# Performance work log

Measured on AMD Instinct MI355X. Metric: run time of the kernel, lower is better.

The kernel has to match this reference:

```python
import jax, jax.numpy as jnp
from jax import lax
import numpy as np

MAX_VAL = 255.0
LEVELS = 5
MS_WEIGHTS = np.array([0.0448, 0.2856, 0.3001, 0.2363, 0.1333], dtype=np.float32)


def _gaussian_window(window_size: int, sigma: float) -> jnp.ndarray:
    # 1D gaussian -> outer product -> [1, 1, ws, ws] conv kernel (channel=1 depthwise)
    x = np.arange(window_size, dtype=np.float64)
    g = np.exp(-((x - window_size // 2) ** 2) / (2.0 * sigma ** 2))
    g = (g / g.sum()).astype(np.float32)
    w2d = np.outer(g, g)
    return jnp.asarray(w2d[None, None, :, :])


def _conv_same(x, win, pad):
    return lax.conv_general_dilated(
        x, win, window_strides=(1, 1), padding=[(pad, pad), (pad, pad)],
        dimension_numbers=('NCHW', 'OIHW', 'NCHW'))


def _ssim_level(img1, img2):
    _, _, w, h = img1.shape
    window_size = min(w, h, 11)
    sigma = 1.5 * window_size / 11
    win = _gaussian_window(window_size, sigma)
    pad = window_size // 2

    mu1 = _conv_same(img1, win, pad)
    mu2 = _conv_same(img2, win, pad)
    mu1_sq = mu1 * mu1
    mu2_sq = mu2 * mu2
    mu1_mu2 = mu1 * mu2
    sigma1_sq = _conv_same(img1 * img1, win, pad) - mu1_sq
    sigma2_sq = _conv_same(img2 * img2, win, pad) - mu2_sq
    sigma12 = _conv_same(img1 * img2, win, pad) - mu1_mu2

    C1 = (0.01 * MAX_VAL) ** 2
    C2 = (0.03 * MAX_VAL) ** 2
    V1 = 2.0 * sigma12 + C2
    V2 = sigma1_sq + sigma2_sq + C2
    ssim_map = (2.0 * mu1_mu2 + C1) * V1 / ((mu1_sq + mu2_sq + C1) * V2)
    mcs_map = V1 / V2
    return ssim_map.mean(), mcs_map.mean()


def _avg_pool2(x):
    b, c, h, w = x.shape
    return x.reshape(b, c, h // 2, 2, w // 2, 2).mean(axis=(3, 5))


def _ms_ssim(img1, img2):
    msssim = []
    mcs = []
    for _ in range(LEVELS):
        s, m = _ssim_level(img1, img2)
        msssim.append(s)
        mcs.append(m)
        img1 = _avg_pool2(img1)
        img2 = _avg_pool2(img2)
    weight = jnp.asarray(MS_WEIGHTS)
    mcs = jnp.stack(mcs)
    value = jnp.prod(mcs[:LEVELS - 1] ** weight[:LEVELS - 1]) * msssim[-1] ** weight[LEVELS - 1]
    return jnp.clip(value / 2.0, 0.0, 1.0)


def setup_inputs() -> dict:
    key = jax.random.key(0)
    k1, k2 = jax.random.split(key)
    shape = (16, 1, 512, 512)
    img1 = jax.random.uniform(k1, shape, dtype=jnp.float32)
    img2 = jax.random.uniform(k2, shape, dtype=jnp.float32)
    return {"img1": img1, "img2": img2}


def reference(img1, img2):
    return _ms_ssim(img1, img2)
```

## Files before the change

### kernel.cpp

```cpp
#include <hip/hip_runtime.h>
#include <hip/hip_fp16.h>
#include <math.h>


#define WS 11
#define TW 64
#define TH 32
#define SROWS 42
#define HSTRIDE 68

__device__ __forceinline__ void gauss_weights(float* w) {
    float s = 0.f;
#pragma unroll
    for (int j = 0; j < WS; ++j) {
        float d = (float)(j - 5);
        float e = expf(-d * d / 4.5f);
        w[j] = e;
        s += e;
    }
    float inv = 1.f / s;
#pragma unroll
    for (int j = 0; j < WS; ++j) w[j] *= inv;
}

__device__ __forceinline__ void h_task(
    int t, const float* __restrict__ p1, const float* __restrict__ p2,
    int W, int x0, int y0, bool interior, const float* w,
    __half2* __restrict__ hSD, __half2* __restrict__ hQ)
{
    int r = t >> 4, xg = t & 15;
    int gy = y0 - 5 + r;
    int gxb = x0 - 8 + 4 * xg;
    float fs[20], fd[20];
    if (interior) {
        const float* r1p = p1 + (size_t)gy * W + gxb;
        const float* r2p = p2 + (size_t)gy * W + gxb;
#pragma unroll
        for (int k = 0; k < 5; ++k) {
            float4 a = *(const float4*)(r1p + 4 * k);
            float4 c = *(const float4*)(r2p + 4 * k);
            fs[4 * k]     = a.x + c.x;  fd[4 * k]     = a.x - c.x;
            fs[4 * k + 1] = a.y + c.y;  fd[4 * k + 1] = a.y - c.y;
            fs[4 * k + 2] = a.z + c.z;  fd[4 * k + 2] = a.z - c.z;
            fs[4 * k + 3] = a.w + c.w;  fd[4 * k + 3] = a.w - c.w;
        }
    } else if (gy >= 0 && gy < W) {
        const float* r1p = p1 + (size_t)gy * W;
        const float* r2p = p2 + (size_t)gy * W;
#pragma unroll
        for (int k = 0; k < 5; ++k) {
            int gx = gxb + 4 * k;
            float4 a = make_float4(0.f, 0.f, 0.f, 0.f);
            float4 c = make_float4(0.f, 0.f, 0.f, 0.f);
            if (gx >= 0 && gx + 3 < W) {
                a = *(const float4*)(r1p + gx);
                c = *(const float4*)(r2p + gx);
            } else if (gx + 3 >= 0 && gx < W) {
                float t1[4] = {0.f, 0.f, 0.f, 0.f};
                float t2[4] = {0.f, 0.f, 0.f, 0.f};
#pragma unroll
                for (int u = 0; u < 4; ++u) {
                    int gxx = gx + u;
                    if (gxx >= 0 && gxx < W) { t1[u] = r1p[gxx]; t2[u] = r2p[gxx]; }
                }
                a = make_float4(t1[0], t1[1], t1[2], t1[3]);
                c = make_float4(t2[0], t2[1], t2[2], t2[3]);
            }
            fs[4 * k]     = a.x + c.x;  fd[4 * k]     = a.x - c.x;
            fs[4 * k + 1] = a.y + c.y;  fd[4 * k + 1] = a.y - c.y;
            fs[4 * k + 2] = a.z + c.z;  fd[4 * k + 2] = a.z - c.z;
            fs[4 * k + 3] = a.w + c.w;  fd[4 * k + 3] = a.w - c.w;
        }
    } else {
#pragma unroll
        for (int k = 0; k < 20; ++k) { fs[k] = 0.f; fd[k] = 0.f; }
    }
    float qs[14], qd[14];
#pragma unroll
    for (int k = 0; k < 14; ++k) {
        qs[k] = fs[k + 3] * fs[k + 3];
        qd[k] = fd[k + 3] * fd[k + 3];
    }
    __half2 outSD[4], outQ[4];
#pragma unroll
    for (int c = 0; c < 4; ++c) {
        float aS = 0.f, aD = 0.f, aS2 = 0.f, aD2 = 0.f;
#pragma unroll
        for (int j = 0; j < WS; ++j) {
            float wj = w[j];
            aS  = fmaf(wj, fs[3 + c + j], aS);
            aD  = fmaf(wj, fd[3 + c + j], aD);
            aS2 = fmaf(wj, qs[c + j], aS2);
            aD2 = fmaf(wj, qd[c + j], aD2);
        }
        outSD[c] = __float22half2_rn(make_float2(aS, aD));
        outQ[c]  = __float22half2_rn(make_float2(aS2, aD2));
    }
    int ho = r * HSTRIDE + 4 * xg;
    *(float4*)&hSD[ho] = *(const float4*)outSD;
    *(float4*)&hQ[ho]  = *(const float4*)outQ;
}

__device__ __forceinline__ void v_phase(
    int W, int x0, int y0, const float* w,
    const __half2* __restrict__ hSD, const __half2* __restrict__ hQ,
    float red[2][4], float* __restrict__ partials, int part_idx)
{
    const int tid = threadIdx.x;
    const int x = tid & 15;
    const int g = tid >> 4;
    float accS[2][4], accD[2][4], accS2[2][4], accD2[2][4];
#pragma unroll
    for (int rr = 0; rr < 2; ++rr)
#pragma unroll
        for (int c = 0; c < 4; ++c) {
            accS[rr][c] = 0.f; accD[rr][c] = 0.f;
            accS2[rr][c] = 0.f; accD2[rr][c] = 0.f;
        }

#pragma unroll
    for (int r = 0; r < 12; ++r) {
        int ho = (2 * g + r) * HSTRIDE + 4 * x;
        float4 rawSD = *(const float4*)&hSD[ho];
        float4 rawQ  = *(const float4*)&hQ[ho];
        const __half2* hpSD = (const __half2*)&rawSD;
        const __half2* hpQ  = (const __half2*)&rawQ;
        float lS[4], lD[4], lS2[4], lD2[4];
#pragma unroll
        for (int c = 0; c < 4; ++c) {
            float2 sd = __half22float2(hpSD[c]);
            float2 q  = __half22float2(hpQ[c]);
            lS[c] = sd.x; lD[c] = sd.y; lS2[c] = q.x; lD2[c] = q.y;
        }
        if (r < 11) {
            float wv = w[r];
#pragma unroll
            for (int c = 0; c < 4; ++c) {
                accS[0][c]  = fmaf(wv, lS[c],  accS[0][c]);
                accD[0][c]  = fmaf(wv, lD[c],  accD[0][c]);
                accS2[0][c] = fmaf(wv, lS2[c], accS2[0][c]);
                accD2[0][c] = fmaf(wv, lD2[c], accD2[0][c]);
            }
        }
        if (r >= 1) {
            float wv = w[r - 1];
#pragma unroll
            for (int c = 0; c < 4; ++c) {
                accS[1][c]  = fmaf(wv, lS[c],  accS[1][c]);
                accD[1][c]  = fmaf(wv, lD[c],  accD[1][c]);
                accS2[1][c] = fmaf(wv, lS2[c], accS2[1][c]);
                accD2[1][c] = fmaf(wv, lD2[c], accD2[1][c]);
            }
        }
    }

    const float C1 = 6.5025f;
    const float C2 = 58.5225f;
    const int Hv = min(TH, W - y0);
    const int Wv = min(TW, W - x0);
    float sacc = 0.f, macc = 0.f;
#pragma unroll
    for (int rr = 0; rr < 2; ++rr) {
        int row = 2 * g + rr;
#pragma unroll
        for (int c = 0; c < 4; ++c) {
            float ms = accS[rr][c], md = accD[rr][c];
            float es = accS2[rr][c], ed = accD2[rr][c];
            float ms2 = ms * ms, md2 = md * md;
            float a  = 0.5f * (ms2 - md2);
            float bb = 0.5f * (ms2 + md2);
            float pq = 0.5f * (es - ed);
            float qq = 0.5f * (es + ed);
            float V1 = (pq - a) + C2;
            float V2 = (qq - bb) + C2;
            float num = a + C1;
            float den = bb + C1;
            float inv = 1.0f / (den * V2);
            float sv = num * V1 * inv;
            float mv = V1 * den * inv;
            if (row < Hv && (4 * x + c) < Wv) { sacc += sv; macc += mv; }
        }
    }

#pragma unroll
    for (int o = 32; o > 0; o >>= 1) {
        sacc += __shfl_down(sacc, o);
        macc += __shfl_down(macc, o);
    }
    int wave = tid >> 6, lane = tid & 63;
    if (lane == 0) { red[0][wave] = sacc; red[1][wave] = macc; }
    __syncthreads();
    if (tid == 0) {
        float s = red[0][0] + red[0][1] + red[0][2] + red[0][3];
        float m = red[1][0] + red[1][1] + red[1][2] + red[1][3];
        partials[2 * part_idx] = s;
        partials[2 * part_idx + 1] = m;
    }
}

__global__ __launch_bounds__(256) void ssim_l0_pool_kernel(
    const float* __restrict__ img1, const float* __restrict__ img2,
    float* __restrict__ l1a, float* __restrict__ l1b,
    float* __restrict__ l2a, float* __restrict__ l2b,
    float* __restrict__ l3a, float* __restrict__ l3b,
    float* __restrict__ l4a, float* __restrict__ l4b,
    float* __restrict__ partials)
{
    __shared__ __half2 hSD[SROWS * HSTRIDE];
    __shared__ __half2 hQ[SROWS * HSTRIDE];
    __shared__ float pl1a[16 * 36];
    __shared__ float pl1b[16 * 36];
    __shared__ float red[2][4];

    const int tid = threadIdx.x;
    const int tx = blockIdx.x, ty = blockIdx.y, b = blockIdx.z;
    const int x0 = tx * TW, y0 = ty * TH;
    const float* p1 = img1 + (size_t)b * 512 * 512;
    const float* p2 = img2 + (size_t)b * 512 * 512;

    float w[WS];
    gauss_weights(w);

    const bool interior = (x0 >= 8) && (x0 <= 512 - 72) && (y0 >= 5) && (y0 <= 512 - 37);

#pragma unroll 1
    for (int t = tid; t < SROWS * 16; t += 256)
        h_task(t, p1, p2, 512, x0, y0, interior, w, hSD, hQ);

#pragma unroll 1
    for (int q = 0; q < 2; ++q) {
        int t = tid + q * 256;
        int r = t >> 5, c = t & 31;
        int gy = y0 + 2 * r, gx = x0 + 2 * c;
        const float* a0 = p1 + (size_t)gy * 512 + gx;
        const float* c0 = p2 + (size_t)gy * 512 + gx;
        float2 u0 = *(const float2*)a0;
        float2 u1 = *(const float2*)(a0 + 512);
        float2 t0 = *(const float2*)c0;
        float2 t1 = *(const float2*)(c0 + 512);
        float v1 = 0.25f * ((u0.x + u0.y) + (u1.x + u1.y));
        float v2 = 0.25f * ((t0.x + t0.y) + (t1.x + t1.y));
        size_t o1 = (size_t)b * 256 * 256 + (size_t)(y0 / 2 + r) * 256 + (x0 / 2 + c);
        l1a[o1] = v1;
        l1b[o1] = v2;
        pl1a[r * 36 + c] = v1;
        pl1b[r * 36 + c] = v2;
    }
    __syncthreads();

    if (tid < 64) {
        int lane = tid;
#pragma unroll
        for (int t = lane; t < 128; t += 64) {
            int r = t >> 4, c = t & 15;
            int R = 2 * r, C = 2 * c;
            float v1 = 0.25f * ((pl1a[R * 36 + C] + pl1a[R * 36 + C + 1]) +
                                (pl1a[(R + 1) * 36 + C] + pl1a[(R + 1) * 36 + C + 1]));
            float v2 = 0.25f * ((pl1b[R * 36 + C] + pl1b[R * 36 + C + 1]) +
                                (pl1b[(R + 1) * 36 + C] + pl1b[(R + 1) * 36 + C + 1]));
            size_t o = (size_t)b * 128 * 128 + (size_t)(y0 / 4 + r) * 128 + (x0 / 4 + c);
            l2a[o] = v1;
            l2b[o] = v2;
        }
        if (lane < 32) {
            int r = lane >> 3, c = lane & 7;
            float q1[2][2], q2[2][2];
#pragma unroll
            for (int i = 0; i < 2; ++i)
#pragma unroll
                for (int j = 0; j < 2; ++j) {
                    int R = 4 * r + 2 * i, C = 4 * c + 2 * j;
                    q1[i][j] = 0.25f * ((pl1a[R * 36 + C] + pl1a[R * 36 + C + 1]) +
                                        (pl1a[(R + 1) * 36 + C] + pl1a[(R + 1) * 36 + C + 1]));
                    q2[i][j] = 0.25f * ((pl1b[R * 36 + C] + pl1b[R * 36 + C + 1]) +
                                        (pl1b[(R + 1) * 36 + C] + pl1b[(R + 1) * 36 + C + 1]));
                }
            float v1 = 0.25f * ((q1[0][0] + q1[0][1]) + (q1[1][0] + q1[1][1]));
            float v2 = 0.25f * ((q2[0][0] + q2[0][1]) + (q2[1][0] + q2[1][1]));
            size_t o = (size_t)b * 64 * 64 + (size_t)(y0 / 8 + r) * 64 + (x0 / 8 + c);
            l3a[o] = v1;
            l3b[o] = v2;
        }
        if (lane < 8) {
            int r = lane >> 2, c = lane & 3;
            float p3a[2][2], p3b[2][2];
#pragma unroll
            for (int i3 = 0; i3 < 2; ++i3)
#pragma unroll
                for (int j3 = 0; j3 < 2; ++j3) {
                    float p2a[2][2], p2b[2][2];
#pragma unroll
                    for (int i2 = 0; i2 < 2; ++i2)
#pragma unroll
                        for (int j2 = 0; j2 < 2; ++j2) {
                            int R = 8 * r + 4 * i3 + 2 * i2;
                            int C = 8 * c + 4 * j3 + 2 * j2;
                            p2a[i2][j2] = 0.25f * ((pl1a[R * 36 + C] + pl1a[R * 36 + C + 1]) +
                                                   (pl1a[(R + 1) * 36 + C] + pl1a[(R + 1) * 36 + C + 1]));
                            p2b[i2][j2] = 0.25f * ((pl1b[R * 36 + C] + pl1b[R * 36 + C + 1]) +
                                                   (pl1b[(R + 1) * 36 + C] + pl1b[(R + 1) * 36 + C + 1]));
                        }
                    p3a[i3][j3] = 0.25f * ((p2a[0][0] + p2a[0][1]) + (p2a[1][0] + p2a[1][1]));
                    p3b[i3][j3] = 0.25f * ((p2b[0][0] + p2b[0][1]) + (p2b[1][0] + p2b[1][1]));
                }
            float v1 = 0.25f * ((p3a[0][0] + p3a[0][1]) + (p3a[1][0] + p3a[1][1]));
            float v2 = 0.25f * ((p3b[0][0] + p3b[0][1]) + (p3b[1][0] + p3b[1][1]));
            size_t o = (size_t)b * 32 * 32 + (size_t)(y0 / 16 + r) * 32 + (x0 / 16 + c);
            l4a[o] = v1;
            l4b[o] = v2;
        }
    }

    int part_idx = ((b * 16 + ty) * 8) + tx;
    v_phase(512, x0, y0, w, hSD, hQ, red, partials, part_idx);
}

__global__ __launch_bounds__(256) void ssim_rest_kernel(
    const float* __restrict__ l1a, const float* __restrict__ l1b,
    const float* __restrict__ l2a, const float* __restrict__ l2b,
    const float* __restrict__ l3a, const float* __restrict__ l3b,
    const float* __restrict__ l4a, const float* __restrict__ l4b,
    float* __restrict__ partials)
{
    __shared__ __half2 hSD[SROWS * HSTRIDE];
    __shared__ __half2 hQ[SROWS * HSTRIDE];
    __shared__ float red[2][4];

    const int tid = threadIdx.x;
    const int lin = blockIdx.x;
    int level, base;
    if (lin < 512)      { level = 1; base = 0; }
    else if (lin < 640) { level = 2; base = 512; }
    else if (lin < 672) { level = 3; base = 640; }
    else                { level = 4; base = 672; }
    const int Wt[4]   = {256, 128, 64, 32};
    const int ntxl[4] = {2, 1, 0, 0};
    const int ntyl[4] = {3, 2, 1, 0};
    const int idx = level - 1;
    const int W = Wt[idx];
    const int li = lin - base;
    const int tx = li & ((1 << ntxl[idx]) - 1);
    const int rem = li >> ntxl[idx];
    const int ty = rem & ((1 << ntyl[idx]) - 1);
    const int b = rem >> ntyl[idx];

    const float* ip1; const float* ip2;
    if (level == 1)      { ip1 = l1a; ip2 = l1b; }
    else if (level == 2) { ip1 = l2a; ip2 = l2b; }
    else if (level == 3) { ip1 = l3a; ip2 = l3b; }
    else                 { ip1 = l4a; ip2 = l4b; }
    const float* p1 = ip1 + (size_t)b * W * W;
    const float* p2 = ip2 + (size_t)b * W * W;

    const int x0 = tx * TW, y0 = ty * TH;

    float w[WS];
    gauss_weights(w);

    const bool interior = (x0 >= 8) && (x0 <= W - 72) && (y0 >= 5) && (y0 <= W - 37);

#pragma unroll 1
    for (int t = tid; t < SROWS * 16; t += 256)
        h_task(t, p1, p2, W, x0, y0, interior, w, hSD, hQ);
    __syncthreads();

    v_phase(W, x0, y0, w, hSD, hQ, red, partials, lin);
}

__global__ __launch_bounds__(256) void finalize_kernel(
    const float* __restrict__ partials, float* __restrict__ out)
{
    __shared__ float lvl_s[5], lvl_m[5];
    __shared__ float red[2][4];
    const int nb[5] = {2048, 512, 128, 32, 16};
    const int off[5] = {0, 2048, 2560, 2688, 2720};
    const float npix[5] = {16.f * 512 * 512, 16.f * 256 * 256, 16.f * 128 * 128,
                           16.f * 64 * 64, 16.f * 32 * 32};
    const int tid = threadIdx.x;

    for (int l = 0; l < 5; ++l) {
        float s = 0.f, m = 0.f;
        for (int i = tid; i < nb[l]; i += 256) {
            s += partials[2 * (off[l] + i)];
            m += partials[2 * (off[l] + i) + 1];
        }
#pragma unroll
        for (int o = 32; o > 0; o >>= 1) {
            s += __shfl_down(s, o);
            m += __shfl_down(m, o);
        }
        int wave = tid >> 6, lane = tid & 63;
        if (lane == 0) { red[0][wave] = s; red[1][wave] = m; }
        __syncthreads();
        if (tid == 0) {
            lvl_s[l] = (red[0][0] + red[0][1] + red[0][2] + red[0][3]) / npix[l];
            lvl_m[l] = (red[1][0] + red[1][1] + red[1][2] + red[1][3]) / npix[l];
        }
        __syncthreads();
    }

    if (tid == 0) {
        const float w[5] = {0.0448f, 0.2856f, 0.3001f, 0.2363f, 0.1333f};
        float v = powf(lvl_m[0], w[0]) * powf(lvl_m[1], w[1]) * powf(lvl_m[2], w[2]) *
                  powf(lvl_m[3], w[3]) * powf(lvl_s[4], w[4]);
        v *= 0.5f;
        v = fminf(fmaxf(v, 0.f), 1.f);
        out[0] = v;
    }
}

extern "C" void kernel_launch(void* const* d_in, const int* in_sizes, int n_in,
                              void* d_out, int out_size, void* d_ws, size_t ws_size,
                              hipStream_t stream) {
    const float* img1 = (const float*)d_in[0];
    const float* img2 = (const float*)d_in[1];
    float* out = (float*)d_out;

    const int B = 16;

    float* wsf = (float*)d_ws;
    float* partials = wsf;
    float* p = wsf + 5472;
    float* l1a = p; p += (size_t)B * 256 * 256;
    float* l1b = p; p += (size_t)B * 256 * 256;
    float* l2a = p; p += (size_t)B * 128 * 128;
    float* l2b = p; p += (size_t)B * 128 * 128;
    float* l3a = p; p += (size_t)B * 64 * 64;
    float* l3b = p; p += (size_t)B * 64 * 64;
    float* l4a = p; p += (size_t)B * 32 * 32;
    float* l4b = p; p += (size_t)B * 32 * 32;

    dim3 block(256);

    ssim_l0_pool_kernel<<<dim3(8, 16, B), block, 0, stream>>>(
        img1, img2, l1a, l1b, l2a, l2b, l3a, l3b, l4a, l4b, partials);

    ssim_rest_kernel<<<dim3(688), block, 0, stream>>>(
        l1a, l1b, l2a, l2b, l3a, l3b, l4a, l4b, partials + 2 * 2048);

    finalize_kernel<<<1, block, 0, stream>>>(partials, out);
}
```

Measured before the change: 130.5 us.

## Stage input halo tiles into LDS with direct global-to-LDS loads

```diff
diff --git a/kernel.cpp b/kernel.cpp
--- a/kernel.cpp
+++ b/kernel.cpp
@@ -7,7 +7,14 @@
 #define TW 64
 #define TH 32
 #define SROWS 42
-#define HSTRIDE 68
+#define SSTRIDE 80
+#define SFLOATS (SROWS * SSTRIDE)
+#define SALLOC 3584
+#define HSTRIDE 64
+#define PL1S 34
+
+typedef const __attribute__((address_space(1))) void gvoid_t;
+typedef __attribute__((address_space(3))) void lvoid_t;
 
 __device__ __forceinline__ void gauss_weights(float* w) {
     float s = 0.f;
@@ -23,57 +30,64 @@
     for (int j = 0; j < WS; ++j) w[j] *= inv;
 }
 
+__device__ __forceinline__ void stage_tile(
+    const float* __restrict__ g1, const float* __restrict__ g2,
+    int H, int W, int x0, int y0,
+    float* __restrict__ s1, float* __restrict__ s2, int tid)
+{
+    const int lane = tid & 63;
+    const int wave = tid >> 6;
+    for (int c = wave; c < 14; c += 4) {
+        int f = c * 256 + lane * 4;
+        int row = f / 80;
+        int col = f - row * 80;
+        int gy = y0 - 5 + row;
+        gy = max(0, min(H - 1, gy));
+        int gx = x0 - 8 + col;
+        gx = max(0, min(W - 4, gx));
+        const float* p1 = g1 + (size_t)gy * W + gx;
+        const float* p2 = g2 + (size_t)gy * W + gx;
+        __builtin_amdgcn_global_load_lds((gvoid_t*)p1, (lvoid_t*)(s1 + f), 16, 0, 0);
+        __builtin_amdgcn_global_load_lds((gvoid_t*)p2, (lvoid_t*)(s2 + f), 16, 0, 0);
+    }
+}
+
+__device__ __forceinline__ void zero_fix(
+    int H, int W, int x0, int y0,
+    float* __restrict__ s1, float* __restrict__ s2, int tid)
+{
+    bool anyOOB = (y0 < 5) || (y0 + 37 > H) || (x0 < 8) || (x0 + 72 > W);
+    if (anyOOB) {
+        for (int t = tid; t < SFLOATS; t += 256) {
+            int r = t / 80, c = t - (t / 80) * 80;
+            int gy = y0 - 5 + r, gx = x0 - 8 + c;
+            if (gy < 0 || gy >= H || gx < 0 || gx >= W) {
+                s1[t] = 0.f;
+                s2[t] = 0.f;
+            }
+        }
+    }
+}
+
 __device__ __forceinline__ void h_task(
-    int t, const float* __restrict__ p1, const float* __restrict__ p2,
-    int W, int x0, int y0, bool interior, const float* w,
-    __half2* __restrict__ hSD, __half2* __restrict__ hQ)
+    int t, const float* __restrict__ s1, const float* __restrict__ s2,
+    const float* w, __half2* __restrict__ hSD, __half2* __restrict__ hQ)
 {
     int r = t >> 4, xg = t & 15;
-    int gy = y0 - 5 + r;
-    int gxb = x0 - 8 + 4 * xg;
+    int sb = r * SSTRIDE + 4 * xg;
+    float f1[20], f2[20];
+#pragma unroll
+    for (int k = 0; k < 5; ++k) {
+        float4 a = *(const float4*)&s1[sb + 4 * k];
+        float4 c = *(const float4*)&s2[sb + 4 * k];
+        f1[4 * k] = a.x; f1[4 * k + 1] = a.y; f1[4 * k + 2] = a.z; f1[4 * k + 3] = a.w;
+        f2[4 * k] = c.x; f2[4 * k + 1] = c.y; f2[4 * k + 2] = c.z; f2[4 * k + 3] = c.w;
+    }
     float fs[20], fd[20];
-    if (interior) {
-        const float* r1p = p1 + (size_t)gy * W + gxb;
-        const float* r2p = p2 + (size_t)gy * W + gxb;
-#pragma unroll
-        for (int k = 0; k < 5; ++k) {
-            float4 a = *(const float4*)(r1p + 4 * k);
-            float4 c = *(const float4*)(r2p + 4 * k);
-            fs[4 * k]     = a.x + c.x;  fd[4 * k]     = a.x - c.x;
-            fs[4 * k + 1] = a.y + c.y;  fd[4 * k + 1] = a.y - c.y;
-            fs[4 * k + 2] = a.z + c.z;  fd[4 * k + 2] = a.z - c.z;
-            fs[4 * k + 3] = a.w + c.w;  fd[4 * k + 3] = a.w - c.w;
-        }
-    } else if (gy >= 0 && gy < W) {
-        const float* r1p = p1 + (size_t)gy * W;
-        const float* r2p = p2 + (size_t)gy * W;
-#pragma unroll
-        for (int k = 0; k < 5; ++k) {
-            int gx = gxb + 4 * k;
-            float4 a = make_float4(0.f, 0.f, 0.f, 0.f);
-            float4 c = make_float4(0.f, 0.f, 0.f, 0.f);
-            if (gx >= 0 && gx + 3 < W) {
-                a = *(const float4*)(r1p + gx);
-                c = *(const float4*)(r2p + gx);
-            } else if (gx + 3 >= 0 && gx < W) {
-                float t1[4] = {0.f, 0.f, 0.f, 0.f};
-                float t2[4] = {0.f, 0.f, 0.f, 0.f};
-#pragma unroll
-                for (int u = 0; u < 4; ++u) {
-                    int gxx = gx + u;
-                    if (gxx >= 0 && gxx < W) { t1[u] = r1p[gxx]; t2[u] = r2p[gxx]; }
-                }
-                a = make_float4(t1[0], t1[1], t1[2], t1[3]);
-                c = make_float4(t2[0], t2[1], t2[2], t2[3]);
-            }
-            fs[4 * k]     = a.x + c.x;  fd[4 * k]     = a.x - c.x;
-            fs[4 * k + 1] = a.y + c.y;  fd[4 * k + 1] = a.y - c.y;
-            fs[4 * k + 2] = a.z + c.z;  fd[4 * k + 2] = a.z - c.z;
-            fs[4 * k + 3] = a.w + c.w;  fd[4 * k + 3] = a.w - c.w;
-        }
-    } else {
-#pragma unroll
-        for (int k = 0; k < 20; ++k) { fs[k] = 0.f; fd[k] = 0.f; }
+#pragma unroll
+    for (int k = 0; k < 20; ++k) {
+        fs[k] = f1[k] + f2[k];
+        fd[k] = f1[k] - f2[k];
     }
     float qs[14], qd[14];
 #pragma unroll
@@ -206,10 +220,12 @@
     float* __restrict__ l4a, float* __restrict__ l4b,
     float* __restrict__ partials)
 {
+    __shared__ float s1[SALLOC];
+    __shared__ float s2[SALLOC];
     __shared__ __half2 hSD[SROWS * HSTRIDE];
     __shared__ __half2 hQ[SROWS * HSTRIDE];
-    __shared__ float pl1a[16 * 36];
-    __shared__ float pl1b[16 * 36];
+    __shared__ float pl1a[16 * PL1S];
+    __shared__ float pl1b[16 * PL1S];
     __shared__ float red[2][4];
 
     const int tid = threadIdx.x;
@@ -218,33 +234,35 @@
     const float* p1 = img1 + (size_t)b * 512 * 512;
     const float* p2 = img2 + (size_t)b * 512 * 512;
 
+    stage_tile(p1, p2, 512, 512, x0, y0, s1, s2, tid);
+
     float w[WS];
     gauss_weights(w);
 
-    const bool interior = (x0 >= 8) && (x0 <= 512 - 72) && (y0 >= 5) && (y0 <= 512 - 37);
+    __syncthreads();
+    zero_fix(512, 512, x0, y0, s1, s2, tid);
+    __syncthreads();
 
 #pragma unroll 1
     for (int t = tid; t < SROWS * 16; t += 256)
-        h_task(t, p1, p2, 512, x0, y0, interior, w, hSD, hQ);
+        h_task(t, s1, s2, w, hSD, hQ);
 
 #pragma unroll 1
     for (int q = 0; q < 2; ++q) {
         int t = tid + q * 256;
         int r = t >> 5, c = t & 31;
-        int gy = y0 + 2 * r, gx = x0 + 2 * c;
-        const float* a0 = p1 + (size_t)gy * 512 + gx;
-        const float* c0 = p2 + (size_t)gy * 512 + gx;
-        float2 u0 = *(const float2*)a0;
-        float2 u1 = *(const float2*)(a0 + 512);
-        float2 t0 = *(const float2*)c0;
-        float2 t1 = *(const float2*)(c0 + 512);
+        int si = (5 + 2 * r) * SSTRIDE + (8 + 2 * c);
+        float2 u0 = *(const float2*)&s1[si];
+        float2 u1 = *(const float2*)&s1[si + SSTRIDE];
+        float2 t0 = *(const float2*)&s2[si];
+        float2 t1 = *(const float2*)&s2[si + SSTRIDE];
         float v1 = 0.25f * ((u0.x + u0.y) + (u1.x + u1.y));
         float v2 = 0.25f * ((t0.x + t0.y) + (t1.x + t1.y));
         size_t o1 = (size_t)b * 256 * 256 + (size_t)(y0 / 2 + r) * 256 + (x0 / 2 + c);
         l1a[o1] = v1;
         l1b[o1] = v2;
-        pl1a[r * 36 + c] = v1;
-        pl1b[r * 36 + c] = v2;
+        pl1a[r * PL1S + c] = v1;
+        pl1b[r * PL1S + c] = v2;
     }
     __syncthreads();
 
@@ -254,10 +272,10 @@
         for (int t = lane; t < 128; t += 64) {
             int r = t >> 4, c = t & 15;
             int R = 2 * r, C = 2 * c;
-            float v1 = 0.25f * ((pl1a[R * 36 + C] + pl1a[R * 36 + C + 1]) +
-                                (pl1a[(R + 1) * 36 + C] + pl1a[(R + 1) * 36 + C + 1]));
-            float v2 = 0.25f * ((pl1b[R * 36 + C] + pl1b[R * 36 + C + 1]) +
-                                (pl1b[(R + 1) * 36 + C] + pl1b[(R + 1) * 36 + C + 1]));
+            float v1 = 0.25f * ((pl1a[R * PL1S + C] + pl1a[R * PL1S + C + 1]) +
+                                (pl1a[(R + 1) * PL1S + C] + pl1a[(R + 1) * PL1S + C + 1]));
+            float v2 = 0.25f * ((pl1b[R * PL1S + C] + pl1b[R * PL1S + C + 1]) +
+                                (pl1b[(R + 1) * PL1S + C] + pl1b[(R + 1) * PL1S + C + 1]));
             size_t o = (size_t)b * 128 * 128 + (size_t)(y0 / 4 + r) * 128 + (x0 / 4 + c);
             l2a[o] = v1;
             l2b[o] = v2;
@@ -270,10 +288,10 @@
 #pragma unroll
                 for (int j = 0; j < 2; ++j) {
                     int R = 4 * r + 2 * i, C = 4 * c + 2 * j;
-                    q1[i][j] = 0.25f * ((pl1a[R * 36 + C] + pl1a[R * 36 + C + 1]) +
-                                        (pl1a[(R + 1) * 36 + C] + pl1a[(R + 1) * 36 + C + 1]));
-                    q2[i][j] = 0.25f * ((pl1b[R * 36 + C] + pl1b[R * 36 + C + 1]) +
-                                        (pl1b[(R + 1) * 36 + C] + pl1b[(R + 1) * 36 + C + 1]));
+                    q1[i][j] = 0.25f * ((pl1a[R * PL1S + C] + pl1a[R * PL1S + C + 1]) +
+                                        (pl1a[(R + 1) * PL1S + C] + pl1a[(R + 1) * PL1S + C + 1]));
+                    q2[i][j] = 0.25f * ((pl1b[R * PL1S + C] + pl1b[R * PL1S + C + 1]) +
+                                        (pl1b[(R + 1) * PL1S + C] + pl1b[(R + 1) * PL1S + C + 1]));
                 }
             float v1 = 0.25f * ((q1[0][0] + q1[0][1]) + (q1[1][0] + q1[1][1]));
             float v2 = 0.25f * ((q2[0][0] + q2[0][1]) + (q2[1][0] + q2[1][1]));
@@ -295,10 +313,10 @@
                         for (int j2 = 0; j2 < 2; ++j2) {
                             int R = 8 * r + 4 * i3 + 2 * i2;
                             int C = 8 * c + 4 * j3 + 2 * j2;
-                            p2a[i2][j2] = 0.25f * ((pl1a[R * 36 + C] + pl1a[R * 36 + C + 1]) +
-                                                   (pl1a[(R + 1) * 36 + C] + pl1a[(R + 1) * 36 + C + 1]));
-                            p2b[i2][j2] = 0.25f * ((pl1b[R * 36 + C] + pl1b[R * 36 + C + 1]) +
-                                                   (pl1b[(R + 1) * 36 + C] + pl1b[(R + 1) * 36 + C + 1]));
+                            p2a[i2][j2] = 0.25f * ((pl1a[R * PL1S + C] + pl1a[R * PL1S + C + 1]) +
+                                                   (pl1a[(R + 1) * PL1S + C] + pl1a[(R + 1) * PL1S + C + 1]));
+                            p2b[i2][j2] = 0.25f * ((pl1b[R * PL1S + C] + pl1b[R * PL1S + C + 1]) +
+                                                   (pl1b[(R + 1) * PL1S + C] + pl1b[(R + 1) * PL1S + C + 1]));
                         }
                     p3a[i3][j3] = 0.25f * ((p2a[0][0] + p2a[0][1]) + (p2a[1][0] + p2a[1][1]));
                     p3b[i3][j3] = 0.25f * ((p2b[0][0] + p2b[0][1]) + (p2b[1][0] + p2b[1][1]));
@@ -322,6 +340,8 @@
     const float* __restrict__ l4a, const float* __restrict__ l4b,
     float* __restrict__ partials)
 {
+    __shared__ float s1[SALLOC];
+    __shared__ float s2[SALLOC];
     __shared__ __half2 hSD[SROWS * HSTRIDE];
     __shared__ __half2 hQ[SROWS * HSTRIDE];
     __shared__ float red[2][4];
@@ -354,14 +374,18 @@
 
     const int x0 = tx * TW, y0 = ty * TH;
 
+    stage_tile(p1, p2, W, W, x0, y0, s1, s2, tid);
+
     float w[WS];
     gauss_weights(w);
 
-    const bool interior = (x0 >= 8) && (x0 <= W - 72) && (y0 >= 5) && (y0 <= W - 37);
+    __syncthreads();
+    zero_fix(W, W, x0, y0, s1, s2, tid);
+    __syncthreads();
 
 #pragma unroll 1
     for (int t = tid; t < SROWS * 16; t += 256)
-        h_task(t, p1, p2, W, x0, y0, interior, w, hSD, hQ);
+        h_task(t, s1, s2, w, hSD, hQ);
     __syncthreads();
 
     v_phase(W, x0, y0, w, hSD, hQ, red, partials, lin);
```

New measurement: 130.3 us. About the same (-0.1%).
